# Optimization experiments

Measured on AMD Instinct MI355X. Metric: run time of the kernel, lower is better.

## Reference

```python
import jax, jax.numpy as jnp
import numpy as np

N_HEADS = 16


def setup_inputs() -> dict:
    key = jax.random.key(0)
    ks = jax.random.split(key, 10)
    B, M, N, C, D = 2, 2048, 2048, 1024, 1024
    s = 0.02
    return {
        "kv": jax.random.normal(ks[0], (B, M, C), jnp.float32),
        "q": jax.random.normal(ks[1], (B, N, D), jnp.float32),
        "Wk": jax.random.normal(ks[2], (C, D), jnp.float32) * s,
        "bk": jnp.zeros((D,), jnp.float32),
        "Wq": jax.random.normal(ks[3], (D, D), jnp.float32) * s,
        "bq": jnp.zeros((D,), jnp.float32),
        "Wv": jax.random.normal(ks[4], (C, D), jnp.float32) * s,
        "bv": jnp.zeros((D,), jnp.float32),
        "Wp": jax.random.normal(ks[5], (D, D), jnp.float32) * s,
        "bp": jnp.zeros((D,), jnp.float32),
    }


def reference(kv, q, Wk, bk, Wq, bq, Wv, bv, Wp, bp):
    B, M, C = kv.shape
    B2, N, D = q.shape
    H = N_HEADS
    hd = D // H
    # projections (weights stored as [in, out]; torch Linear is x @ W.T + b with W [out,in])
    k = (kv @ Wk + bk).reshape(B, M, H, hd).transpose(0, 2, 1, 3)  # [B,H,M,hd]
    qh = (q @ Wq + bq).reshape(B, N, H, hd).transpose(0, 2, 1, 3)  # [B,H,N,hd]
    v = (kv @ Wv + bv).reshape(B, M, H, hd).transpose(0, 2, 1, 3)  # [B,H,M,hd]
    scale = 1.0 / jnp.sqrt(jnp.asarray(hd, k.dtype))
    att = jnp.einsum("bhnd,bhmd->bhnm", qh, k) * scale
    att = jax.nn.softmax(att, axis=-1)
    y = jnp.einsum("bhnm,bhmd->bhnd", att, v)  # [B,H,N,hd]
    y = y.transpose(0, 2, 1, 3).reshape(B, N, D)
    return y @ Wp + bp
```

## Files before the change

### kernel.cpp

```cpp
#include <hip/hip_runtime.h>

#define DV 1024
#define HD 64

typedef short v4s __attribute__((ext_vector_type(4)));
typedef short v8s __attribute__((ext_vector_type(8)));
typedef float v4f __attribute__((ext_vector_type(4)));
typedef int   v2i __attribute__((ext_vector_type(2)));

__device__ __forceinline__ short f2bf(float x){
  unsigned u = __float_as_uint(x);
  u += 0x7FFFu + ((u >> 16) & 1u);
  return (short)(u >> 16);
}

__device__ __forceinline__ int swz(int lane){
  return (((lane & 7) ^ (lane >> 3)) << 3);
}

__global__ __launch_bounds__(256) void cvt2(const float* __restrict__ xa,
                                            const float* __restrict__ xb,
                                            short* __restrict__ ya,
                                            short* __restrict__ yb, int n){
  const float* x = blockIdx.y ? xb : xa;
  short* y = blockIdx.y ? yb : ya;
  int stride = gridDim.x * 256 * 4;
  for (int i = (blockIdx.x * 256 + threadIdx.x) * 4; i < n; i += stride){
    float4 v = *(const float4*)(x + i);
    v4s s; s.x = f2bf(v.x); s.y = f2bf(v.y); s.z = f2bf(v.z); s.w = f2bf(v.w);
    *(v4s*)(y + i) = s;
  }
}

__global__ __launch_bounds__(256) void tcvt4(
    const float* __restrict__ W0, const float* __restrict__ W1,
    const float* __restrict__ W2, const float* __restrict__ W3,
    short* __restrict__ T0, short* __restrict__ T1,
    short* __restrict__ T2, short* __restrict__ T3){
  const float* W; short* Wt;
  switch (blockIdx.z){
    case 0: W = W0; Wt = T0; break;
    case 1: W = W1; Wt = T1; break;
    case 2: W = W2; Wt = T2; break;
    default: W = W3; Wt = T3; break;
  }
  __shared__ short L[64 * 68];
  const int t = threadIdx.x;
  const int k0 = blockIdx.y * 64, n0 = blockIdx.x * 64;
  const int rr = t >> 4, cc = (t & 15) * 4;
  #pragma unroll
  for (int j = 0; j < 4; j++){
    int r = rr + j * 16;
    float4 v = *(const float4*)(W + (size_t)(k0 + r) * DV + n0 + cc);
    v4s s; s.x = f2bf(v.x); s.y = f2bf(v.y); s.z = f2bf(v.z); s.w = f2bf(v.w);
    *(v4s*)&L[r * 68 + cc] = s;
  }
  __syncthreads();
  #pragma unroll
  for (int j = 0; j < 4; j++){
    int n = rr + j * 16;
    v4s s;
    s.x = L[(cc + 0) * 68 + n];
    s.y = L[(cc + 1) * 68 + n];
    s.z = L[(cc + 2) * 68 + n];
    s.w = L[(cc + 3) * 68 + n];
    *(v4s*)(Wt + (size_t)(n0 + n) * DV + k0 + cc) = s;
  }
}

template<typename OUT_T>
__device__ __forceinline__ void gemm_tile(
    const short* __restrict__ A, const short* __restrict__ Bt,
    const float* __restrict__ bias, OUT_T* __restrict__ C,
    int M, int N, int K, float out_scale, int m0, int n0, bool bias_row)
{
  __shared__ short As[128 * 64];
  __shared__ short Bs[128 * 64];
  const int tid = threadIdx.x;
  const int wave = tid >> 6, lane = tid & 63;
  const int quad = lane >> 4, l15 = lane & 15;
  const int wr = (wave >> 1) * 64, wc = (wave & 1) * 64;
  const int srow = lane >> 3;
  const int sw = swz(lane);
  const v4f vzero = {0.f, 0.f, 0.f, 0.f};

  const short* pa[4]; const short* pb[4];
  #pragma unroll
  for (int ii = 0; ii < 4; ii++){
    int i = wave * 4 + ii;
    pa[ii] = A  + (size_t)(m0 + i * 8 + srow) * K + sw;
    pb[ii] = Bt + (size_t)(n0 + i * 8 + srow) * K + sw;
  }

  v8s ra[4], rb[4];
  #pragma unroll
  for (int ii = 0; ii < 4; ii++){
    ra[ii] = *(const v8s*)(pa[ii]);
    rb[ii] = *(const v8s*)(pb[ii]);
  }

  v4f acc[4][4];
  #pragma unroll
  for (int i = 0; i < 4; i++)
    #pragma unroll
    for (int j = 0; j < 4; j++)
      acc[i][j] = vzero;

  for (int kt = 0; kt < K; kt += 64){
    __syncthreads();
    #pragma unroll
    for (int ii = 0; ii < 4; ii++){
      int i = wave * 4 + ii;
      *(v8s*)&As[i * 512 + lane * 8] = ra[ii];
      *(v8s*)&Bs[i * 512 + lane * 8] = rb[ii];
    }
    __syncthreads();
    if (kt + 64 < K){
      #pragma unroll
      for (int ii = 0; ii < 4; ii++){
        ra[ii] = *(const v8s*)(pa[ii] + kt + 64);
        rb[ii] = *(const v8s*)(pb[ii] + kt + 64);
      }
    }
    #pragma unroll
    for (int ks = 0; ks < 2; ks++){
      v8s a[4], b[4];
      #pragma unroll
      for (int mt = 0; mt < 4; mt++)
        a[mt] = *(const v8s*)&As[(wr + mt * 16 + l15) * 64 + (((ks * 4 + quad) ^ (l15 & 7)) << 3)];
      #pragma unroll
      for (int nt = 0; nt < 4; nt++)
        b[nt] = *(const v8s*)&Bs[(wc + nt * 16 + l15) * 64 + (((ks * 4 + quad) ^ (l15 & 7)) << 3)];
      #pragma unroll
      for (int mt = 0; mt < 4; mt++)
        #pragma unroll
        for (int nt = 0; nt < 4; nt++)
          acc[mt][nt] = __builtin_amdgcn_mfma_f32_16x16x32_bf16(a[mt], b[nt], acc[mt][nt], 0, 0, 0);
    }
  }

  #pragma unroll
  for (int mt = 0; mt < 4; mt++){
    #pragma unroll
    for (int nt = 0; nt < 4; nt++){
      int row = m0 + wr + mt * 16 + quad * 4;
      int col = n0 + wc + nt * 16 + l15;
      float bcol = bias_row ? 0.0f : bias[col];
      #pragma unroll
      for (int r = 0; r < 4; r++){
        float bv = bias_row ? bias[row + r] : bcol;
        float v = (acc[mt][nt][r] + bv) * out_scale;
        if (sizeof(OUT_T) == 2)
          ((short*)C)[(size_t)(row + r) * N + col] = f2bf(v);
        else
          ((float*)C)[(size_t)(row + r) * N + col] = v;
      }
    }
  }
}

__global__ __launch_bounds__(256, 3) void proj3(
    const short* __restrict__ qb, const short* __restrict__ kvb,
    const short* __restrict__ Wqt, const short* __restrict__ Wkt,
    const short* __restrict__ Wvt,
    const float* __restrict__ bq, const float* __restrict__ bk,
    const float* __restrict__ bv,
    short* __restrict__ Qp, short* __restrict__ Kp, short* __restrict__ VT,
    float qscale)
{
  int bid = blockIdx.x;
  const short *A, *Bt; const float* bias; short* C;
  int M, N, m0, n0; float scale; bool brow;
  if (bid < 512){
    int z = bid >> 8, l = bid & 255;
    M = 4096; N = 1024; m0 = (l & 31) * 128; n0 = (l >> 5) * 128;
    A = z ? kvb : qb; Bt = z ? Wkt : Wqt; bias = z ? bk : bq;
    C = z ? Kp : Qp; scale = z ? 1.0f : qscale; brow = false;
  } else {
    int l = bid - 512;
    M = 1024; N = 4096; m0 = (l >> 5) * 128; n0 = (l & 31) * 128;
    A = Wvt; Bt = kvb; bias = bv; C = VT; scale = 1.0f; brow = true;
  }
  gemm_tile<short>(A, Bt, bias, C, M, N, 1024, scale, m0, n0, brow);
}

__global__ __launch_bounds__(256, 2) void gemm_f32(
    const short* __restrict__ A, const short* __restrict__ Bt,
    const float* __restrict__ bias, float* __restrict__ C)
{
  __shared__ short As[128 * 64];
  __shared__ short Bs[64 * 64];
  const int tid = threadIdx.x;
  const int wave = tid >> 6, lane = tid & 63;
  const int quad = lane >> 4, l15 = lane & 15;
  const int bid = blockIdx.x;
  const int m0 = (bid & 31) * 128, n0 = (bid >> 5) * 64;
  const int wr = (wave >> 1) * 64, wc = (wave & 1) * 32;
  const int srow = lane >> 3;
  const int sw = swz(lane);
  const int K = 1024;
  const v4f vzero = {0.f, 0.f, 0.f, 0.f};

  const short* pa[4]; const short* pb[2];
  #pragma unroll
  for (int ii = 0; ii < 4; ii++)
    pa[ii] = A + (size_t)(m0 + (wave * 4 + ii) * 8 + srow) * K + sw;
  #pragma unroll
  for (int ii = 0; ii < 2; ii++)
    pb[ii] = Bt + (size_t)(n0 + (wave * 2 + ii) * 8 + srow) * K + sw;

  v8s ra[4], rb[2];
  #pragma unroll
  for (int ii = 0; ii < 4; ii++) ra[ii] = *(const v8s*)(pa[ii]);
  #pragma unroll
  for (int ii = 0; ii < 2; ii++) rb[ii] = *(const v8s*)(pb[ii]);

  v4f acc[4][2];
  #pragma unroll
  for (int i = 0; i < 4; i++){ acc[i][0] = vzero; acc[i][1] = vzero; }

  for (int kt = 0; kt < K; kt += 64){
    __syncthreads();
    #pragma unroll
    for (int ii = 0; ii < 4; ii++)
      *(v8s*)&As[(wave * 4 + ii) * 512 + lane * 8] = ra[ii];
    #pragma unroll
    for (int ii = 0; ii < 2; ii++)
      *(v8s*)&Bs[(wave * 2 + ii) * 512 + lane * 8] = rb[ii];
    __syncthreads();
    if (kt + 64 < K){
      #pragma unroll
      for (int ii = 0; ii < 4; ii++) ra[ii] = *(const v8s*)(pa[ii] + kt + 64);
      #pragma unroll
      for (int ii = 0; ii < 2; ii++) rb[ii] = *(const v8s*)(pb[ii] + kt + 64);
    }
    #pragma unroll
    for (int ks = 0; ks < 2; ks++){
      v8s a[4], b[2];
      #pragma unroll
      for (int mt = 0; mt < 4; mt++)
        a[mt] = *(const v8s*)&As[(wr + mt * 16 + l15) * 64 + (((ks * 4 + quad) ^ (l15 & 7)) << 3)];
      #pragma unroll
      for (int nt = 0; nt < 2; nt++)
        b[nt] = *(const v8s*)&Bs[(wc + nt * 16 + l15) * 64 + (((ks * 4 + quad) ^ (l15 & 7)) << 3)];
      #pragma unroll
      for (int mt = 0; mt < 4; mt++)
        #pragma unroll
        for (int nt = 0; nt < 2; nt++)
          acc[mt][nt] = __builtin_amdgcn_mfma_f32_16x16x32_bf16(a[mt], b[nt], acc[mt][nt], 0, 0, 0);
    }
  }

  #pragma unroll
  for (int mt = 0; mt < 4; mt++){
    #pragma unroll
    for (int nt = 0; nt < 2; nt++){
      int row = m0 + wr + mt * 16 + quad * 4;
      int col = n0 + wc + nt * 16 + l15;
      float bcol = bias[col];
      #pragma unroll
      for (int r = 0; r < 4; r++)
        C[(size_t)(row + r) * 1024 + col] = acc[mt][nt][r] + bcol;
    }
  }
}

__global__ __launch_bounds__(256, 3) void attn(
    const short* __restrict__ Qp, const short* __restrict__ Kp,
    const short* __restrict__ Vt, short* __restrict__ Y)
{
  __shared__ short Ks[64 * 64];
  __shared__ short Vs[64 * 68];
  const int tid = threadIdx.x;
  const int wave = tid >> 6, lane = tid & 63;
  const int quad = lane >> 4, l15 = lane & 15;
  const int gid = blockIdx.x;
  const int qi = gid >> 5, bh = gid & 31;
  const int h = bh & 15, b = bh >> 4;
  const int n0 = qi * 128;
  const int srow = lane >> 3;
  const int c8 = (lane & 7) * 8;
  const int sw = swz(lane);
  const size_t rowbase = (size_t)b * 2048;
  const v4f vzero = {0.f, 0.f, 0.f, 0.f};

  v8s qf[2][2];
  #pragma unroll
  for (int qt = 0; qt < 2; qt++){
    const short* qrow = Qp + (rowbase + n0 + wave * 32 + qt * 16 + l15) * DV + h * HD + quad * 8;
    qf[qt][0] = *(const v8s*)(qrow);
    qf[qt][1] = *(const v8s*)(qrow + 32);
  }

  const short* pk[2]; const short* pv[2];
  #pragma unroll
  for (int ii = 0; ii < 2; ii++){
    int i = wave * 2 + ii;
    pk[ii] = Kp + (rowbase + i * 8 + srow) * DV + h * HD + sw;
    pv[ii] = Vt + (size_t)(h * HD + i * 8 + srow) * 4096 + rowbase + c8;
  }
  v8s rk[2], rv[2];
  #pragma unroll
  for (int ii = 0; ii < 2; ii++){ rk[ii] = *(const v8s*)(pk[ii]); rv[ii] = *(const v8s*)(pv[ii]); }

  v4f o[4][2];
  #pragma unroll
  for (int dt = 0; dt < 4; dt++){ o[dt][0] = vzero; o[dt][1] = vzero; }
  float lsum[2] = {0.0f, 0.0f};

  for (int kt = 0; kt < 32; kt++){
    __syncthreads();
    #pragma unroll
    for (int ii = 0; ii < 2; ii++){
      int i = wave * 2 + ii;
      *(v8s*)&Ks[i * 512 + lane * 8] = rk[ii];
      *(v8s*)&Vs[(i * 8 + srow) * 68 + c8] = rv[ii];
    }
    __syncthreads();
    if (kt < 31){
      #pragma unroll
      for (int ii = 0; ii < 2; ii++){
        rk[ii] = *(const v8s*)(pk[ii] + (size_t)(kt + 1) * 64 * DV);
        rv[ii] = *(const v8s*)(pv[ii] + (kt + 1) * 64);
      }
    }

    v4f s[2][4];
    #pragma unroll
    for (int qt = 0; qt < 2; qt++)
      #pragma unroll
      for (int kvt = 0; kvt < 4; kvt++) s[qt][kvt] = vzero;
    #pragma unroll
    for (int ks = 0; ks < 2; ks++){
      v8s a[4];
      #pragma unroll
      for (int kvt = 0; kvt < 4; kvt++)
        a[kvt] = *(const v8s*)&Ks[(kvt * 16 + l15) * 64 + (((ks * 4 + quad) ^ (l15 & 7)) << 3)];
      #pragma unroll
      for (int kvt = 0; kvt < 4; kvt++)
        #pragma unroll
        for (int qt = 0; qt < 2; qt++)
          s[qt][kvt] = __builtin_amdgcn_mfma_f32_16x16x32_bf16(a[kvt], qf[qt][ks], s[qt][kvt], 0, 0, 0);
    }

    v4s pf[2][4];
    #pragma unroll
    for (int qt = 0; qt < 2; qt++)
      #pragma unroll
      for (int kvt = 0; kvt < 4; kvt++){
        float p0 = __builtin_amdgcn_exp2f(s[qt][kvt][0]);
        float p1 = __builtin_amdgcn_exp2f(s[qt][kvt][1]);
        float p2 = __builtin_amdgcn_exp2f(s[qt][kvt][2]);
        float p3 = __builtin_amdgcn_exp2f(s[qt][kvt][3]);
        lsum[qt] += (p0 + p1) + (p2 + p3);
        unsigned u0 = __float_as_uint(p0) + 0x8000u;
        unsigned u1 = __float_as_uint(p1) + 0x8000u;
        unsigned u2 = __float_as_uint(p2) + 0x8000u;
        unsigned u3 = __float_as_uint(p3) + 0x8000u;
        v2i pi;
        pi.x = (int)__builtin_amdgcn_perm(u1, u0, 0x07060302u);
        pi.y = (int)__builtin_amdgcn_perm(u3, u2, 0x07060302u);
        pf[qt][kvt] = __builtin_bit_cast(v4s, pi);
      }

    #pragma unroll
    for (int ks = 0; ks < 4; ks++){
      v4s a[4];
      #pragma unroll
      for (int dt = 0; dt < 4; dt++)
        a[dt] = *(const v4s*)&Vs[(dt * 16 + l15) * 68 + ks * 16 + quad * 4];
      #pragma unroll
      for (int dt = 0; dt < 4; dt++)
        #pragma unroll
        for (int qt = 0; qt < 2; qt++)
          o[dt][qt] = __builtin_amdgcn_mfma_f32_16x16x16bf16_1k(a[dt], pf[qt][ks], o[dt][qt], 0, 0, 0);
    }
  }

  #pragma unroll
  for (int qt = 0; qt < 2; qt++){
    float ls = lsum[qt];
    ls += __shfl_xor(ls, 16);
    ls += __shfl_xor(ls, 32);
    float inv = 1.0f / ls;
    size_t row = rowbase + n0 + wave * 32 + qt * 16 + l15;
    #pragma unroll
    for (int dt = 0; dt < 4; dt++){
      int col = h * HD + dt * 16 + quad * 4;
      unsigned p0 = (unsigned short)f2bf(o[dt][qt][0] * inv) |
                    ((unsigned)(unsigned short)f2bf(o[dt][qt][1] * inv) << 16);
      unsigned p1 = (unsigned short)f2bf(o[dt][qt][2] * inv) |
                    ((unsigned)(unsigned short)f2bf(o[dt][qt][3] * inv) << 16);
      *(unsigned*)(Y + row * DV + col)     = p0;
      *(unsigned*)(Y + row * DV + col + 2) = p1;
    }
  }
}

extern "C" void kernel_launch(void* const* d_in, const int* in_sizes, int n_in,
                              void* d_out, int out_size, void* d_ws, size_t ws_size,
                              hipStream_t stream) {
  const float* kv = (const float*)d_in[0];
  const float* q  = (const float*)d_in[1];
  const float* Wk = (const float*)d_in[2];
  const float* bk = (const float*)d_in[3];
  const float* Wq = (const float*)d_in[4];
  const float* bq = (const float*)d_in[5];
  const float* Wv = (const float*)d_in[6];
  const float* bv = (const float*)d_in[7];
  const float* Wp = (const float*)d_in[8];
  const float* bp = (const float*)d_in[9];

  const size_t E  = 4194304;
  const size_t WE = 1048576;
  short* p   = (short*)d_ws;
  short* kvb = p; p += E;
  short* qb  = p; p += E;
  short* Wkt = p; p += WE;
  short* Wqt = p; p += WE;
  short* Wvt = p; p += WE;
  short* Wpt = p; p += WE;
  short* Kp  = p; p += E;
  short* Qp  = p; p += E;
  short* VT  = p; p += E;
  short* Yb  = p; p += E;

  cvt2<<<dim3(512, 2), 256, 0, stream>>>(kv, q, kvb, qb, (int)E);
  tcvt4<<<dim3(16, 16, 4), 256, 0, stream>>>(Wk, Wq, Wv, Wp, Wkt, Wqt, Wvt, Wpt);

  proj3<<<768, 256, 0, stream>>>(qb, kvb, Wqt, Wkt, Wvt, bq, bk, bv,
                                 Qp, Kp, VT, 0.18033688011f);

  attn<<<512, 256, 0, stream>>>(Qp, Kp, VT, Yb);

  gemm_f32<<<512, 256, 0, stream>>>(Yb, Wpt, bp, (float*)d_out);
}
```

Baseline: 204.8 us.

## Split attention KV range across wave pairs with double-buffered async K loads

Restructures the attention kernel so each wave handles 64 query rows over half of the KV sequence (split-K across wave pairs), with partial outputs and row sums combined through shared memory at the end. K tiles are loaded straight into LDS with global_load_lds and double buffered, which removes one barrier per iteration. V still goes through registers but is prefetched two tiles ahead. The cost is more accumulator registers and LDS, so occupancy drops from 3 to 2 blocks per CU, and a reduction epilogue is added.

After: 212.0 us. 1.04x slower.

```diff
diff --git a/kernel.cpp b/kernel.cpp
--- a/kernel.cpp
+++ b/kernel.cpp
@@ -12,6 +12,11 @@
   unsigned u = __float_as_uint(x);
   u += 0x7FFFu + ((u >> 16) & 1u);
   return (short)(u >> 16);
+}
+
+__device__ __forceinline__ void async16(const void* g, void* l){
+  __builtin_amdgcn_global_load_lds((const __attribute__((address_space(1))) void*)g,
+                                   (__attribute__((address_space(3))) void*)l, 16, 0, 0);
 }
 
 __device__ __forceinline__ int swz(int lane){
@@ -265,15 +270,16 @@
   }
 }
 
-__global__ __launch_bounds__(256, 3) void attn(
+__global__ __launch_bounds__(256, 2) void attn(
     const short* __restrict__ Qp, const short* __restrict__ Kp,
     const short* __restrict__ Vt, short* __restrict__ Y)
 {
-  __shared__ short Ks[64 * 64];
-  __shared__ short Vs[64 * 68];
+  __shared__ short Ks[2][2][64 * 64];
+  __shared__ short Vs[2][2][64 * 68];
   const int tid = threadIdx.x;
   const int wave = tid >> 6, lane = tid & 63;
   const int quad = lane >> 4, l15 = lane & 15;
+  const int qh = wave & 1, kh = wave >> 1;
   const int gid = blockIdx.x;
   const int qi = gid >> 5, bh = gid & 31;
   const int h = bh & 15, b = bh >> 4;
@@ -282,52 +288,64 @@
   const int c8 = (lane & 7) * 8;
   const int sw = swz(lane);
   const size_t rowbase = (size_t)b * 2048;
+  const size_t kvbase = rowbase + (size_t)kh * 1024;
   const v4f vzero = {0.f, 0.f, 0.f, 0.f};
 
-  v8s qf[2][2];
-  #pragma unroll
-  for (int qt = 0; qt < 2; qt++){
-    const short* qrow = Qp + (rowbase + n0 + wave * 32 + qt * 16 + l15) * DV + h * HD + quad * 8;
+  v8s qf[4][2];
+  #pragma unroll
+  for (int qt = 0; qt < 4; qt++){
+    const short* qrow = Qp + (rowbase + n0 + qh * 64 + qt * 16 + l15) * DV + h * HD + quad * 8;
     qf[qt][0] = *(const v8s*)(qrow);
     qf[qt][1] = *(const v8s*)(qrow + 32);
   }
 
-  const short* pk[2]; const short* pv[2];
-  #pragma unroll
-  for (int ii = 0; ii < 2; ii++){
-    int i = wave * 2 + ii;
-    pk[ii] = Kp + (rowbase + i * 8 + srow) * DV + h * HD + sw;
-    pv[ii] = Vt + (size_t)(h * HD + i * 8 + srow) * 4096 + rowbase + c8;
-  }
-  v8s rk[2], rv[2];
-  #pragma unroll
-  for (int ii = 0; ii < 2; ii++){ rk[ii] = *(const v8s*)(pk[ii]); rv[ii] = *(const v8s*)(pv[ii]); }
-
-  v4f o[4][2];
-  #pragma unroll
-  for (int dt = 0; dt < 4; dt++){ o[dt][0] = vzero; o[dt][1] = vzero; }
-  float lsum[2] = {0.0f, 0.0f};
-
-  for (int kt = 0; kt < 32; kt++){
-    __syncthreads();
-    #pragma unroll
-    for (int ii = 0; ii < 2; ii++){
-      int i = wave * 2 + ii;
-      *(v8s*)&Ks[i * 512 + lane * 8] = rk[ii];
-      *(v8s*)&Vs[(i * 8 + srow) * 68 + c8] = rv[ii];
-    }
-    __syncthreads();
-    if (kt < 31){
-      #pragma unroll
-      for (int ii = 0; ii < 2; ii++){
-        rk[ii] = *(const v8s*)(pk[ii] + (size_t)(kt + 1) * 64 * DV);
-        rv[ii] = *(const v8s*)(pv[ii] + (kt + 1) * 64);
-      }
-    }
-
-    v4f s[2][4];
-    #pragma unroll
-    for (int qt = 0; qt < 2; qt++)
+  const short* pkg[4];  const short* pv[4];
+  #pragma unroll
+  for (int c = 0; c < 4; c++){
+    int r = qh * 32 + c * 8 + srow;
+    pkg[c] = Kp + (kvbase + r) * DV + h * HD + sw;
+    pv[c]  = Vt + (size_t)(h * HD + r) * 4096 + kvbase + c8;
+  }
+
+  v8s rv[4];
+  #pragma unroll
+  for (int c = 0; c < 4; c++){
+    async16(pkg[c], &Ks[kh][0][(qh * 32 + c * 8) * 64]);
+    rv[c] = *(const v8s*)(pv[c]);
+  }
+  #pragma unroll
+  for (int c = 0; c < 4; c++)
+    *(v8s*)&Vs[kh][0][(qh * 32 + c * 8 + srow) * 68 + c8] = rv[c];
+  #pragma unroll
+  for (int c = 0; c < 4; c++)
+    rv[c] = *(const v8s*)(pv[c] + 64);
+  __syncthreads();
+
+  v4f o[4][4];
+  #pragma unroll
+  for (int dt = 0; dt < 4; dt++)
+    #pragma unroll
+    for (int qt = 0; qt < 4; qt++) o[dt][qt] = vzero;
+  float lsum[4] = {0.f, 0.f, 0.f, 0.f};
+
+  for (int t = 0; t < 16; t++){
+    const int cur = t & 1, nxt = cur ^ 1;
+    if (t < 15){
+      #pragma unroll
+      for (int c = 0; c < 4; c++){
+        async16(pkg[c] + (size_t)(t + 1) * 64 * DV, &Ks[kh][nxt][(qh * 32 + c * 8) * 64]);
+        *(v8s*)&Vs[kh][nxt][(qh * 32 + c * 8 + srow) * 68 + c8] = rv[c];
+      }
+      if (t < 14){
+        #pragma unroll
+        for (int c = 0; c < 4; c++)
+          rv[c] = *(const v8s*)(pv[c] + (t + 2) * 64);
+      }
+    }
+
+    v4f s[4][4];
+    #pragma unroll
+    for (int qt = 0; qt < 4; qt++)
       #pragma unroll
       for (int kvt = 0; kvt < 4; kvt++) s[qt][kvt] = vzero;
     #pragma unroll
@@ -335,23 +353,23 @@
       v8s a[4];
       #pragma unroll
       for (int kvt = 0; kvt < 4; kvt++)
-        a[kvt] = *(const v8s*)&Ks[(kvt * 16 + l15) * 64 + (((ks * 4 + quad) ^ (l15 & 7)) << 3)];
+        a[kvt] = *(const v8s*)&Ks[kh][cur][(kvt * 16 + l15) * 64 + (((ks * 4 + quad) ^ (l15 & 7)) << 3)];
       #pragma unroll
       for (int kvt = 0; kvt < 4; kvt++)
         #pragma unroll
-        for (int qt = 0; qt < 2; qt++)
+        for (int qt = 0; qt < 4; qt++)
           s[qt][kvt] = __builtin_amdgcn_mfma_f32_16x16x32_bf16(a[kvt], qf[qt][ks], s[qt][kvt], 0, 0, 0);
     }
 
-    v4s pf[2][4];
-    #pragma unroll
-    for (int qt = 0; qt < 2; qt++)
-      #pragma unroll
-      for (int kvt = 0; kvt < 4; kvt++){
-        float p0 = __builtin_amdgcn_exp2f(s[qt][kvt][0]);
-        float p1 = __builtin_amdgcn_exp2f(s[qt][kvt][1]);
-        float p2 = __builtin_amdgcn_exp2f(s[qt][kvt][2]);
-        float p3 = __builtin_amdgcn_exp2f(s[qt][kvt][3]);
+    #pragma unroll
+    for (int ks = 0; ks < 4; ks++){
+      v4s pfq[4];
+      #pragma unroll
+      for (int qt = 0; qt < 4; qt++){
+        float p0 = __builtin_amdgcn_exp2f(s[qt][ks][0]);
+        float p1 = __builtin_amdgcn_exp2f(s[qt][ks][1]);
+        float p2 = __builtin_amdgcn_exp2f(s[qt][ks][2]);
+        float p3 = __builtin_amdgcn_exp2f(s[qt][ks][3]);
         lsum[qt] += (p0 + p1) + (p2 + p3);
         unsigned u0 = __float_as_uint(p0) + 0x8000u;
         unsigned u1 = __float_as_uint(p1) + 0x8000u;
@@ -360,39 +378,61 @@
         v2i pi;
         pi.x = (int)__builtin_amdgcn_perm(u1, u0, 0x07060302u);
         pi.y = (int)__builtin_amdgcn_perm(u3, u2, 0x07060302u);
-        pf[qt][kvt] = __builtin_bit_cast(v4s, pi);
-      }
-
-    #pragma unroll
-    for (int ks = 0; ks < 4; ks++){
+        pfq[qt] = __builtin_bit_cast(v4s, pi);
+      }
       v4s a[4];
       #pragma unroll
       for (int dt = 0; dt < 4; dt++)
-        a[dt] = *(const v4s*)&Vs[(dt * 16 + l15) * 68 + ks * 16 + quad * 4];
+        a[dt] = *(const v4s*)&Vs[kh][cur][(dt * 16 + l15) * 68 + ks * 16 + quad * 4];
       #pragma unroll
       for (int dt = 0; dt < 4; dt++)
         #pragma unroll
-        for (int qt = 0; qt < 2; qt++)
-          o[dt][qt] = __builtin_amdgcn_mfma_f32_16x16x16bf16_1k(a[dt], pf[qt][ks], o[dt][qt], 0, 0, 0);
-    }
-  }
-
-  #pragma unroll
-  for (int qt = 0; qt < 2; qt++){
-    float ls = lsum[qt];
-    ls += __shfl_xor(ls, 16);
-    ls += __shfl_xor(ls, 32);
-    float inv = 1.0f / ls;
-    size_t row = rowbase + n0 + wave * 32 + qt * 16 + l15;
-    #pragma unroll
-    for (int dt = 0; dt < 4; dt++){
-      int col = h * HD + dt * 16 + quad * 4;
-      unsigned p0 = (unsigned short)f2bf(o[dt][qt][0] * inv) |
-                    ((unsigned)(unsigned short)f2bf(o[dt][qt][1] * inv) << 16);
-      unsigned p1 = (unsigned short)f2bf(o[dt][qt][2] * inv) |
-                    ((unsigned)(unsigned short)f2bf(o[dt][qt][3] * inv) << 16);
-      *(unsigned*)(Y + row * DV + col)     = p0;
-      *(unsigned*)(Y + row * DV + col + 2) = p1;
+        for (int qt = 0; qt < 4; qt++)
+          o[dt][qt] = __builtin_amdgcn_mfma_f32_16x16x16bf16_1k(a[dt], pfq[qt], o[dt][qt], 0, 0, 0);
+    }
+    __syncthreads();
+  }
+
+  float* sm = (float*)&Ks[0][0][0];
+  float* sl = (float*)&Vs[0][0][0];
+  if (kh == 1){
+    float* base = sm + qh * 4096;
+    #pragma unroll
+    for (int dt = 0; dt < 4; dt++)
+      #pragma unroll
+      for (int qt = 0; qt < 4; qt++)
+        *(v4f*)(base + (dt * 4 + qt) * 256 + lane * 4) = o[dt][qt];
+    v4f lv = {lsum[0], lsum[1], lsum[2], lsum[3]};
+    *(v4f*)(sl + qh * 256 + lane * 4) = lv;
+  }
+  __syncthreads();
+  if (kh == 0){
+    float* base = sm + qh * 4096;
+    v4f lv = *(const v4f*)(sl + qh * 256 + lane * 4);
+    float inv[4];
+    #pragma unroll
+    for (int qt = 0; qt < 4; qt++){
+      float ls = lsum[qt] + lv[qt];
+      ls += __shfl_xor(ls, 16);
+      ls += __shfl_xor(ls, 32);
+      inv[qt] = 1.0f / ls;
+    }
+    #pragma unroll
+    for (int qt = 0; qt < 4; qt++){
+      size_t row = rowbase + n0 + qh * 64 + qt * 16 + l15;
+      #pragma unroll
+      for (int dt = 0; dt < 4; dt++){
+        v4f ov = *(const v4f*)(base + (dt * 4 + qt) * 256 + lane * 4);
+        float y0 = (o[dt][qt][0] + ov[0]) * inv[qt];
+        float y1 = (o[dt][qt][1] + ov[1]) * inv[qt];
+        float y2 = (o[dt][qt][2] + ov[2]) * inv[qt];
+        float y3 = (o[dt][qt][3] + ov[3]) * inv[qt];
+        int col = h * HD + dt * 16 + quad * 4;
+        unsigned p0 = (unsigned short)f2bf(y0) | ((unsigned)(unsigned short)f2bf(y1) << 16);
+        unsigned p1 = (unsigned short)f2bf(y2) | ((unsigned)(unsigned short)f2bf(y3) << 16);
+        *(unsigned*)(Y + row * DV + col)     = p0;
+        *(unsigned*)(Y + row * DV + col + 2) = p1;
+      }
     }
   }
 }
```
